# Optimization experiments

Measured on AMD Instinct MI355X. Metric: run time of the kernel, lower is better.

The kernel has to match this reference:

```python
import jax, jax.numpy as jnp
import numpy as np

N = 4096
IN_F = 256
HEADS = 8
OUT_F = 64  # per-head dim
NEG_BIG = -9e15


def setup_inputs() -> dict:
    key = jax.random.key(0)
    k1, k2, k3, k4 = jax.random.split(key, 4)
    x = jax.random.normal(k1, (N, IN_F), dtype=jnp.float32)
    adj = jax.random.randint(k2, (N, N), 0, 2, dtype=jnp.int32)
    # linear weight (no bias): torch Linear(in, heads*out) -> store as [in, heads*out]
    lim_w = float(np.sqrt(6.0 / (IN_F + HEADS * OUT_F)))
    W = jax.random.uniform(k3, (IN_F, HEADS * OUT_F), minval=-lim_w, maxval=lim_w, dtype=jnp.float32)
    # attn param [1, heads, 2*out], xavier_uniform
    lim_a = float(np.sqrt(6.0 / (HEADS + 2 * OUT_F)))
    attn = jax.random.uniform(k4, (1, HEADS, 2 * OUT_F), minval=-lim_a, maxval=lim_a, dtype=jnp.float32)
    return {"x": x, "adj": adj, "W": W, "attn": attn}


def reference(x, adj, W, attn):
    n = x.shape[0]
    H = attn.shape[1]
    D = attn.shape[2] // 2
    h = (x @ W).reshape(n, H, D)                       # [N, H, D]
    a_src = attn[0, :, :D]                             # [H, D]
    a_dst = attn[0, :, D:]                             # [H, D]
    # separable GAT score: e[i, j, h] = a_src.h_i + a_dst.h_j
    s_src = jnp.einsum('nhd,hd->nh', h, a_src)         # [N, H]
    s_dst = jnp.einsum('nhd,hd->nh', h, a_dst)         # [N, H]
    e = s_src[:, None, :] + s_dst[None, :, :]          # [N, N, H]
    e = jnp.where(adj[:, :, None] > 0, e, jnp.float32(NEG_BIG))
    attention = jax.nn.softmax(e, axis=1)              # softmax over neighbor dim j
    h_prime = jnp.einsum('ijh,jhd->ihd', attention, h)  # [N, H, D]
    return h_prime.reshape(n, H * D)
```

## Files before the change

### kernel.cpp

```cpp
#include <hip/hip_runtime.h>
#include <hip/hip_bf16.h>
#include <stdint.h>

typedef __attribute__((ext_vector_type(4))) float  f32x4;
typedef __attribute__((ext_vector_type(8))) short  s16x8;
typedef __attribute__((ext_vector_type(4))) int    i32x4;
typedef __attribute__((ext_vector_type(4))) unsigned int u32x4;

#define NN 4096
#define GT_LD 4096
#define NUM_STRIDE (4096 * 512)

__device__ __forceinline__ unsigned short f2bf(float f) {
  uint32_t u = __builtin_bit_cast(uint32_t, f);
  u += 0x7FFF + ((u >> 16) & 1);
  return (unsigned short)(u >> 16);
}

__device__ __forceinline__ void gload_lds16(const void* g, void* l) {
  __builtin_amdgcn_global_load_lds(
      (const __attribute__((address_space(1))) unsigned int*)g,
      (__attribute__((address_space(3))) unsigned int*)l, 16, 0, 0);
}

__global__ __launch_bounds__(512) void k_small(const float* __restrict__ x,
                                               const float* __restrict__ W,
                                               unsigned short* __restrict__ xb,
                                               unsigned short* __restrict__ wt) {
  int bid = blockIdx.x;
  if (bid < 512) {
    int t = bid * 512 + threadIdx.x;
    f32x4 v = ((const f32x4*)x)[t];
    uint64_t r = (uint64_t)f2bf(v.x) | ((uint64_t)f2bf(v.y) << 16) |
                 ((uint64_t)f2bf(v.z) << 32) | ((uint64_t)f2bf(v.w) << 48);
    ((uint64_t*)xb)[t] = r;
  } else {
    int t = (bid - 512) * 512 + threadIdx.x;
    int c = t >> 8, k = t & 255;
    wt[t] = f2bf(W[k * 512 + c]);
  }
}

__global__ __launch_bounds__(512) void k_fat(const int* __restrict__ adj,
                                             unsigned int* __restrict__ bits,
                                             const unsigned short* __restrict__ xb,
                                             const unsigned short* __restrict__ wt,
                                             const float* __restrict__ attn,
                                             unsigned short* __restrict__ gt) {
  __shared__ unsigned short lx[16 * 256];
  __shared__ unsigned short lw[512 * 64];

  if (blockIdx.x >= 256) {
    int row = blockIdx.x - 256;
    int t = threadIdx.x;
    const i32x4* ap = (const i32x4*)(adj + row * 4096) + 2 * t;
    i32x4 v0 = ap[0], v1 = ap[1];
    unsigned b = (v0.x ? 1u : 0u) | (v0.y ? 2u : 0u) |
                 (v0.z ? 4u : 0u) | (v0.w ? 8u : 0u) |
                 (v1.x ? 16u : 0u) | (v1.y ? 32u : 0u) |
                 (v1.z ? 64u : 0u) | (v1.w ? 128u : 0u);
    ((unsigned char*)bits)[row * 512 + t] = (unsigned char)b;
    return;
  }

  const int tid = threadIdx.x;
  const int lane = tid & 63;
  const int h = tid >> 6;
  const int l15 = lane & 15, lg = lane >> 4;
  const int j0 = blockIdx.x * 16;

  {
    int L = tid * 16;
    int row = L >> 9, b = L & 511;
    int sb = b ^ ((row & 7) << 4);
    gload_lds16((const char*)xb + (j0 + row) * 512 + sb, (char*)lx + L);
  }

  f32x4 acc[4] = {};
  for (int kc = 0; kc < 4; ++kc) {
#pragma unroll
    for (int i = 0; i < 8; ++i) {
      int L = (i * 512 + tid) * 16;
      int c = L >> 7, b = L & 127;
      int sb = b ^ ((c & 7) << 4);
      gload_lds16((const char*)wt + c * 512 + kc * 128 + sb, (char*)lw + L);
    }
    asm volatile("s_waitcnt vmcnt(0)");
    __syncthreads();
#pragma unroll
    for (int kk = 0; kk < 2; ++kk) {
      int kby = kk * 64 + lg * 16;
      s16x8 a = *(const s16x8*)((const char*)lx + l15 * 512 +
                                ((kc * 128 + kby) ^ ((l15 & 7) << 4)));
#pragma unroll
      for (int n = 0; n < 4; ++n) {
        int c = h * 64 + n * 16 + l15;
        s16x8 b = *(const s16x8*)((const char*)lw + c * 128 + (kby ^ ((c & 7) << 4)));
        acc[n] = __builtin_amdgcn_mfma_f32_16x16x32_bf16(a, b, acc[n], 0, 0, 0);
      }
    }
    __syncthreads();
  }

  float adv[4];
#pragma unroll
  for (int n = 0; n < 4; ++n) adv[n] = attn[h * 128 + 64 + n * 16 + l15];
#pragma unroll
  for (int r = 0; r < 4; ++r) {
    float p = acc[0][r] * adv[0] + acc[1][r] * adv[1] +
              acc[2][r] * adv[2] + acc[3][r] * adv[3];
#pragma unroll
    for (int m = 1; m < 16; m <<= 1) p += __shfl_xor(p, m);
    float w = expf(p);
    int node = j0 + lg * 4 + r;
#pragma unroll
    for (int n = 0; n < 4; ++n) {
      int c = h * 64 + n * 16 + l15;
      gt[c * GT_LD + node] = f2bf(acc[n][r] * w);
    }
    if (l15 == 0) gt[(512 + h) * GT_LD + node] = f2bf(w);
  }
}

__global__ __launch_bounds__(256, 3) void k_gemm(const unsigned int* __restrict__ bits,
                                                 const unsigned short* __restrict__ GT,
                                                 float* __restrict__ out,
                                                 float* __restrict__ numx,
                                                 float* __restrict__ den,
                                                 int klen) {
  __shared__ unsigned short lA[128 * 64];
  __shared__ unsigned short lB[128 * 64];
  const int tid = threadIdx.x;
  const int lane = tid & 63, wid = tid >> 6;
  const int wr = wid >> 1, wc = wid & 1;
  const int l15 = lane & 15, lg = lane >> 4;

  int g = blockIdx.x;
  int swz = (g & 7) * 20 + (g >> 3);
  int bx = swz / 5, by = swz % 5;
  const int row0 = bx * 128, c0 = by * 128;

  const int s = blockIdx.y;
  float* num = (s == 0) ? out : (numx + (s - 1) * NUM_STRIDE);
  float* dens = den + s * (4096 * 8);

  const int r = tid >> 1, hf = tid & 1;
  const unsigned int* bitrow = bits + (row0 + r) * 128 + s * (klen >> 5) + hf;

  const char* Bbase = (const char*)GT + c0 * 8192 + (long)s * klen * 2;

  auto stageB = [&](int kt) {
#pragma unroll
    for (int i = 0; i < 4; ++i) {
      int L = (i * 256 + tid) * 16;
      int rr = L >> 7, b = L & 127;
      int sb = b ^ ((rr & 7) << 4);
      gload_lds16(Bbase + rr * 8192 + kt * 128 + sb, (char*)lB + L);
    }
  };
  auto expandA = [&](uint32_t m) {
#pragma unroll
    for (int q = 0; q < 4; ++q) {
      u32x4 w;
#pragma unroll
      for (int d = 0; d < 4; ++d) {
        int b = q * 8 + d * 2;
        w[d] = ((m >> b) & 1u) * 0x3F80u + ((m >> (b + 1)) & 1u) * 0x3F800000u;
      }
      int byte = (hf * 64 + q * 16) ^ ((r & 7) << 4);
      *(u32x4*)((char*)lA + r * 128 + byte) = w;
    }
  };

  f32x4 acc[4][4] = {};
  const int NKT = klen >> 6;

  uint32_t m = bitrow[0];
  for (int kt = 0; kt < NKT; ++kt) {
    uint32_t m2 = (kt < NKT - 1) ? bitrow[(kt + 1) * 2] : 0;
    stageB(kt);
    expandA(m);
    __syncthreads();
#pragma unroll
    for (int kk = 0; kk < 2; ++kk) {
      int kby = kk * 64 + lg * 16;
      s16x8 a[4], b[4];
#pragma unroll
      for (int mm = 0; mm < 4; ++mm) {
        int rr = wr * 64 + mm * 16 + l15;
        a[mm] = *(const s16x8*)((const char*)lA + rr * 128 + (kby ^ ((rr & 7) << 4)));
      }
#pragma unroll
      for (int n = 0; n < 4; ++n) {
        int c = wc * 64 + n * 16 + l15;
        b[n] = *(const s16x8*)((const char*)lB + c * 128 + (kby ^ ((c & 7) << 4)));
      }
#pragma unroll
      for (int mm = 0; mm < 4; ++mm)
#pragma unroll
        for (int n = 0; n < 4; ++n)
          acc[mm][n] = __builtin_amdgcn_mfma_f32_16x16x32_bf16(a[mm], b[n], acc[mm][n], 0, 0, 0);
    }
    m = m2;
    __syncthreads();
  }

#pragma unroll
  for (int mm = 0; mm < 4; ++mm)
#pragma unroll
    for (int n = 0; n < 4; ++n) {
      int c = c0 + wc * 64 + n * 16 + l15;
#pragma unroll
      for (int rr = 0; rr < 4; ++rr) {
        int i = row0 + wr * 64 + mm * 16 + lg * 4 + rr;
        float v = acc[mm][n][rr];
        if (c < 512) num[i * 512 + c] = v;
        else if (c < 520) dens[i * 8 + (c - 512)] = v;
      }
    }
}

__global__ __launch_bounds__(256) void k_final(float* __restrict__ out,
                                               const float* __restrict__ numx,
                                               const float* __restrict__ den,
                                               int S) {
  int t = blockIdx.x * 256 + threadIdx.x;
  int i = t >> 7, h = (t >> 4) & 7;
  f32x4 v = ((const f32x4*)out)[t];
  float d = den[i * 8 + h];
  for (int s = 1; s < S; ++s) {
    f32x4 u = ((const f32x4*)(numx + (s - 1) * NUM_STRIDE))[t];
    v.x += u.x; v.y += u.y; v.z += u.z; v.w += u.w;
    d += den[s * 4096 * 8 + i * 8 + h];
  }
  v.x /= d; v.y /= d; v.z /= d; v.w /= d;
  ((f32x4*)out)[t] = v;
}

extern "C" void kernel_launch(void* const* d_in, const int* in_sizes, int n_in,
                              void* d_out, int out_size, void* d_ws, size_t ws_size,
                              hipStream_t stream) {
  const float* x    = (const float*)d_in[0];
  const int*   adj  = (const int*)d_in[1];
  const float* W    = (const float*)d_in[2];
  const float* attn = (const float*)d_in[3];
  float* out = (float*)d_out;
  char* ws = (char*)d_ws;

  unsigned int*   BITS = (unsigned int*)(ws);
  unsigned short* GTp  = (unsigned short*)(ws + 2097152);
  unsigned short* XB   = (unsigned short*)(ws + 6815744);
  unsigned short* WT   = (unsigned short*)(ws + 8912896);
  float*          DEN  = (float*)(ws + 9175040);
  float*          NUMX = (float*)(ws + 9699328);

  int S = 1;
  if (ws_size >= 9699328ull + 3ull * NUM_STRIDE * 4 + 65536) S = 4;
  else if (ws_size >= 9699328ull + 1ull * NUM_STRIDE * 4 + 65536) S = 2;

  k_small<<<768, 512, 0, stream>>>(x, W, XB, WT);
  k_fat  <<<4352, 512, 0, stream>>>(adj, BITS, XB, WT, attn, GTp);
  dim3 ggrid(160, S);
  k_gemm <<<ggrid, 256, 0, stream>>>(BITS, GTp, out, NUMX, DEN, 4096 / S);
  k_final<<<2048, 256, 0, stream>>>(out, NUMX, DEN, S);
}
```

Before: 67.29 us.

## Double-buffer B tile in LDS and prefetch next k-tile during MFMA

Adds a second LDS buffer for the B (GT) tile so the direct-to-LDS global loads for the next k-tile are issued before the current tile is computed. Full __syncthreads are replaced by explicit partial vmcnt waits and raw s_barrier, which lets the next tile's loads stay in flight. s_setprio is raised around the MFMA block. The kernel uses more LDS, which may limit residency under the 3-block launch bound, and the hand-written waitcnt counts must match the number of outstanding loads.

```diff
diff --git a/kernel.cpp b/kernel.cpp
--- a/kernel.cpp
+++ b/kernel.cpp
@@ -129,7 +129,7 @@
                                                  float* __restrict__ den,
                                                  int klen) {
   __shared__ unsigned short lA[128 * 64];
-  __shared__ unsigned short lB[128 * 64];
+  __shared__ unsigned short lB[2][128 * 64];
   const int tid = threadIdx.x;
   const int lane = tid & 63, wid = tid >> 6;
   const int wr = wid >> 1, wc = wid & 1;
@@ -149,13 +149,13 @@
 
   const char* Bbase = (const char*)GT + c0 * 8192 + (long)s * klen * 2;
 
-  auto stageB = [&](int kt) {
+  auto stageB = [&](unsigned short* dst, int kt) {
 #pragma unroll
     for (int i = 0; i < 4; ++i) {
       int L = (i * 256 + tid) * 16;
       int rr = L >> 7, b = L & 127;
       int sb = b ^ ((rr & 7) << 4);
-      gload_lds16(Bbase + rr * 8192 + kt * 128 + sb, (char*)lB + L);
+      gload_lds16(Bbase + rr * 8192 + kt * 128 + sb, (char*)dst + L);
     }
   };
   auto expandA = [&](uint32_t m) {
@@ -175,12 +175,25 @@
   f32x4 acc[4][4] = {};
   const int NKT = klen >> 6;
 
+  stageB(lB[0], 0);
   uint32_t m = bitrow[0];
+
   for (int kt = 0; kt < NKT; ++kt) {
-    uint32_t m2 = (kt < NKT - 1) ? bitrow[(kt + 1) * 2] : 0;
-    stageB(kt);
+    int cur = kt & 1;
+    uint32_t m2 = 0;
+    if (kt < NKT - 1) {
+      stageB(lB[cur ^ 1], kt + 1);
+      m2 = bitrow[(kt + 1) * 2];
+    }
     expandA(m);
-    __syncthreads();
+    if (kt < NKT - 1)
+      asm volatile("s_waitcnt vmcnt(5) lgkmcnt(0)" ::: "memory");
+    else
+      asm volatile("s_waitcnt vmcnt(0) lgkmcnt(0)" ::: "memory");
+    __builtin_amdgcn_sched_barrier(0);
+    __builtin_amdgcn_s_barrier();
+
+    __builtin_amdgcn_s_setprio(1);
 #pragma unroll
     for (int kk = 0; kk < 2; ++kk) {
       int kby = kk * 64 + lg * 16;
@@ -193,7 +206,7 @@
 #pragma unroll
       for (int n = 0; n < 4; ++n) {
         int c = wc * 64 + n * 16 + l15;
-        b[n] = *(const s16x8*)((const char*)lB + c * 128 + (kby ^ ((c & 7) << 4)));
+        b[n] = *(const s16x8*)((const char*)lB[cur] + c * 128 + (kby ^ ((c & 7) << 4)));
       }
 #pragma unroll
       for (int mm = 0; mm < 4; ++mm)
@@ -201,8 +214,12 @@
         for (int n = 0; n < 4; ++n)
           acc[mm][n] = __builtin_amdgcn_mfma_f32_16x16x32_bf16(a[mm], b[n], acc[mm][n], 0, 0, 0);
     }
+    __builtin_amdgcn_s_setprio(0);
+
+    asm volatile("s_waitcnt lgkmcnt(0)" ::: "memory");
+    __builtin_amdgcn_sched_barrier(0);
+    __builtin_amdgcn_s_barrier();
     m = m2;
-    __syncthreads();
   }
 
 #pragma unroll
```

New measurement: 68.70 us. 1.02x slower.

## Triple-buffer B tiles in LDS and expand adjacency bits directly into registers

Applied to the files above, without the earlier changes.

The GEMM kernel now keeps three LDS buffers for the GT operand and prefetches the next k-tile asynchronously while computing the current one, using one barrier per iteration instead of two. The A operand (adjacency mask expanded to bf16 0/1) is no longer written to and read back from LDS. Each lane loads the 64-bit mask words for its own rows and builds the MFMA A fragments in registers. This removes LDS traffic and a sync for A and overlaps global loads with MFMA, at the cost of more LDS (three B buffers) and more VGPRs, which may lower occupancy.

```diff
diff --git a/kernel.cpp b/kernel.cpp
--- a/kernel.cpp
+++ b/kernel.cpp
@@ -128,12 +128,14 @@
                                                  float* __restrict__ numx,
                                                  float* __restrict__ den,
                                                  int klen) {
-  __shared__ unsigned short lA[128 * 64];
-  __shared__ unsigned short lB[128 * 64];
+  __shared__ unsigned short lB0[128 * 64];
+  __shared__ unsigned short lB1[128 * 64];
+  __shared__ unsigned short lB2[128 * 64];
   const int tid = threadIdx.x;
   const int lane = tid & 63, wid = tid >> 6;
   const int wr = wid >> 1, wc = wid & 1;
   const int l15 = lane & 15, lg = lane >> 4;
+  const int lg8 = lg * 8;
 
   int g = blockIdx.x;
   int swz = (g & 7) * 20 + (g >> 3);
@@ -144,65 +146,78 @@
   float* num = (s == 0) ? out : (numx + (s - 1) * NUM_STRIDE);
   float* dens = den + s * (4096 * 8);
 
-  const int r = tid >> 1, hf = tid & 1;
-  const unsigned int* bitrow = bits + (row0 + r) * 128 + s * (klen >> 5) + hf;
+  const uint64_t* ap[4];
+#pragma unroll
+  for (int m = 0; m < 4; ++m)
+    ap[m] = (const uint64_t*)((const char*)bits +
+            (size_t)(row0 + wr * 64 + m * 16 + l15) * 512 + (size_t)s * (klen >> 3));
 
   const char* Bbase = (const char*)GT + c0 * 8192 + (long)s * klen * 2;
 
-  auto stageB = [&](int kt) {
+  auto stageB = [&](unsigned short* dst, int kt) {
 #pragma unroll
     for (int i = 0; i < 4; ++i) {
       int L = (i * 256 + tid) * 16;
       int rr = L >> 7, b = L & 127;
       int sb = b ^ ((rr & 7) << 4);
-      gload_lds16(Bbase + rr * 8192 + kt * 128 + sb, (char*)lB + L);
-    }
-  };
-  auto expandA = [&](uint32_t m) {
-#pragma unroll
-    for (int q = 0; q < 4; ++q) {
-      u32x4 w;
-#pragma unroll
-      for (int d = 0; d < 4; ++d) {
-        int b = q * 8 + d * 2;
-        w[d] = ((m >> b) & 1u) * 0x3F80u + ((m >> (b + 1)) & 1u) * 0x3F800000u;
-      }
-      int byte = (hf * 64 + q * 16) ^ ((r & 7) << 4);
-      *(u32x4*)((char*)lA + r * 128 + byte) = w;
+      gload_lds16(Bbase + rr * 8192 + kt * 128 + sb, (char*)dst + L);
     }
   };
 
   f32x4 acc[4][4] = {};
   const int NKT = klen >> 6;
 
-  uint32_t m = bitrow[0];
+  unsigned short *pR = lB0, *pS = lB1, *pF = lB2;
+
+  stageB(pR, 0);
+  uint64_t Wc[4];
+#pragma unroll
+  for (int m = 0; m < 4; ++m) Wc[m] = ap[m][0];
+
   for (int kt = 0; kt < NKT; ++kt) {
-    uint32_t m2 = (kt < NKT - 1) ? bitrow[(kt + 1) * 2] : 0;
-    stageB(kt);
-    expandA(m);
-    __syncthreads();
+    uint64_t Wn[4] = {0, 0, 0, 0};
+    if (kt < NKT - 1) {
+      stageB(pS, kt + 1);
+#pragma unroll
+      for (int m = 0; m < 4; ++m) Wn[m] = ap[m][kt + 1];
+      asm volatile("s_waitcnt vmcnt(8)" ::: "memory");
+    } else {
+      asm volatile("s_waitcnt vmcnt(0)" ::: "memory");
+    }
+    __builtin_amdgcn_s_barrier();
+    __builtin_amdgcn_sched_barrier(0);
+
 #pragma unroll
     for (int kk = 0; kk < 2; ++kk) {
+      s16x8 af[4];
+#pragma unroll
+      for (int m = 0; m < 4; ++m) {
+        uint32_t part = (uint32_t)(Wc[m] >> (kk * 32));
+        uint32_t byte = (part >> lg8) & 0xFFu;
+        u32x4 w;
+#pragma unroll
+        for (int d = 0; d < 4; ++d)
+          w[d] = ((byte >> (2 * d)) & 1u) * 0x3F80u +
+                 ((byte >> (2 * d + 1)) & 1u) * 0x3F800000u;
+        af[m] = __builtin_bit_cast(s16x8, w);
+      }
       int kby = kk * 64 + lg * 16;
-      s16x8 a[4], b[4];
-#pragma unroll
-      for (int mm = 0; mm < 4; ++mm) {
-        int rr = wr * 64 + mm * 16 + l15;
-        a[mm] = *(const s16x8*)((const char*)lA + rr * 128 + (kby ^ ((rr & 7) << 4)));
-      }
+      s16x8 b[4];
 #pragma unroll
       for (int n = 0; n < 4; ++n) {
         int c = wc * 64 + n * 16 + l15;
-        b[n] = *(const s16x8*)((const char*)lB + c * 128 + (kby ^ ((c & 7) << 4)));
-      }
-#pragma unroll
-      for (int mm = 0; mm < 4; ++mm)
+        b[n] = *(const s16x8*)((const char*)pR + c * 128 + (kby ^ ((c & 7) << 4)));
+      }
+#pragma unroll
+      for (int m = 0; m < 4; ++m)
 #pragma unroll
         for (int n = 0; n < 4; ++n)
-          acc[mm][n] = __builtin_amdgcn_mfma_f32_16x16x32_bf16(a[mm], b[n], acc[mm][n], 0, 0, 0);
-    }
-    m = m2;
-    __syncthreads();
+          acc[m][n] = __builtin_amdgcn_mfma_f32_16x16x32_bf16(af[m], b[n], acc[m][n], 0, 0, 0);
+    }
+
+    unsigned short* t = pR; pR = pS; pS = pF; pF = t;
+#pragma unroll
+    for (int m = 0; m < 4; ++m) Wc[m] = Wn[m];
   }
 
 #pragma unroll
```

Measured after the change: 75.78 us. +12.6%, slower.
